# Optimization experiments

Hardware: AMD Instinct MI355X
Metric: run time of the kernel (lower is better)

The kernel has to match this reference:

```python
import jax, jax.numpy as jnp
import numpy as np

# RPNTrainingProposal / RpnTrainingModel constants (defaults in source)
POS_IOU_T = 0.7
NEG_IOU_T = 0.3
TOTAL_SAMPLES = 256
MAX_POS = 128
CLS_W = 1.0
REG_W = 2.0


def pairwise_iou(a, b):
    # a: [N,4], b: [M,4], boxes as (x1, y1, x2, y2) -> [N, M]
    area_a = (a[:, 2] - a[:, 0]) * (a[:, 3] - a[:, 1])
    area_b = (b[:, 2] - b[:, 0]) * (b[:, 3] - b[:, 1])
    lt = jnp.maximum(a[:, None, :2], b[None, :, :2])
    rb = jnp.minimum(a[:, None, 2:], b[None, :, 2:])
    wh = jnp.clip(rb - lt, 0.0)
    inter = wh[..., 0] * wh[..., 1]
    return inter / (area_a[:, None] + area_b[None, :] - inter)


def encode_bbox(anchors, gt):
    aw = anchors[:, 2] - anchors[:, 0]
    ah = anchors[:, 3] - anchors[:, 1]
    acx = anchors[:, 0] + 0.5 * aw
    acy = anchors[:, 1] + 0.5 * ah
    gw = gt[:, 2] - gt[:, 0]
    gh = gt[:, 3] - gt[:, 1]
    gcx = gt[:, 0] + 0.5 * gw
    gcy = gt[:, 1] + 0.5 * gh
    return jnp.stack([(gcx - acx) / aw, (gcy - acy) / ah,
                      jnp.log(gw / aw), jnp.log(gh / ah)], axis=1)


def select_training_samples(anchors, gt_bboxes):
    """Static-shape port of RPNTrainingProposal.call.

    Faithful to the source: 'max_scores' is argmax(iou, axis=1) (an int gt
    index) which the source compares against the float iou thresholds, so
    label=1 <=> gt_idx >= 1 and label=0 <=> gt_idx == 0. top_k(max_scores, n_pos)
    therefore selects exactly the label==1 anchors (and top_k(-max_scores) the
    label==0 ones); tf.random_shuffle subsampling is replaced by a
    deterministic (stable index-order) subsample of the same sets.
    """
    iou = pairwise_iou(anchors, gt_bboxes)                  # [N, M]
    gt_idx = jnp.argmax(iou, axis=1).astype(jnp.int32)      # source 'max_scores'
    ms = gt_idx.astype(jnp.float32)
    labels = jnp.full(gt_idx.shape, -1, jnp.int32)
    labels = jnp.where(ms > POS_IOU_T, 1, labels)
    labels = jnp.where(ms < NEG_IOU_T, 0, labels)
    pos_mask = labels == 1
    neg_mask = labels == 0
    num_pos = jnp.sum(pos_mask)
    cur_pos = jnp.minimum(num_pos, MAX_POS)                 # negatives fill the rest
    # stable sort keys: positives (resp. negatives) first, in anchor-index order
    pos_order = jnp.argsort(jnp.where(pos_mask, 0, 1), stable=True)
    neg_order = jnp.argsort(jnp.where(neg_mask, 0, 1), stable=True)
    i = jnp.arange(TOTAL_SAMPLES)
    sel = jnp.where(i < cur_pos, pos_order[i],
                    neg_order[jnp.clip(i - cur_pos, 0)])    # [256]
    return sel, labels[sel], gt_idx[sel]


def reference(rpn_score, rpn_bboxes_txtytwth, anchors, gt_bboxes):
    sel, sel_labels, sel_gt_idx = select_training_samples(anchors, gt_bboxes)
    # classification loss: sparse softmax cross-entropy, mean over samples
    logp = jax.nn.log_softmax(rpn_score[sel], axis=-1)      # [256, 2]
    cls = -jnp.take_along_axis(logp, sel_labels[:, None].astype(jnp.int32), axis=1)
    rpn_cls_loss = CLS_W * jnp.mean(cls)
    t_gt = encode_bbox(anchors[sel], gt_bboxes[sel_gt_idx])  # [256, 4]
    t_pred = rpn_bboxes_txtytwth[sel]
    inside = sel_labels.astype(t_pred.dtype)[:, None]
    d = inside * (t_pred - t_gt)
    ad = jnp.abs(d)
    sm = jnp.where(ad < 1.0, 0.5 * d * d, ad - 0.5)
    rpn_reg_loss = jnp.mean(jnp.sum(REG_W * sm, axis=1))
    return rpn_cls_loss, rpn_reg_loss


def setup_inputs() -> dict:
    key = jax.random.key(0)
    ks = jax.random.split(key, 10)
    N, M = 300000, 100

    def make_boxes(kcx, kcy, kw, kh, n, img=1000.0):
        cx = jax.random.uniform(kcx, (n,)) * img
        cy = jax.random.uniform(kcy, (n,)) * img
        w = jax.random.uniform(kw, (n,)) * 120.0 + 16.0
        h = jax.random.uniform(kh, (n,)) * 120.0 + 16.0
        return jnp.stack([cx - 0.5 * w, cy - 0.5 * h, cx + 0.5 * w, cy + 0.5 * h], axis=1)

    anchors = make_boxes(ks[0], ks[1], ks[2], ks[3], N)
    gt_bboxes = make_boxes(ks[4], ks[5], ks[6], ks[7], M)
    rpn_score = jax.random.normal(ks[8], (N, 2), jnp.float32)
    rpn_bboxes_txtytwth = jax.random.normal(ks[9], (N, 4), jnp.float32) * 0.1
    return {"rpn_score": rpn_score, "rpn_bboxes_txtytwth": rpn_bboxes_txtytwth,
            "anchors": anchors, "gt_bboxes": gt_bboxes}
```

## Files before the change

### kernel.cpp

```cpp
#include <hip/hip_runtime.h>
#include <math.h>

#define MAXGT 128
#define POS_LIMIT 128
#define TOTAL 256


__global__ void __launch_bounds__(256)
k1_argmax(const float* __restrict__ anchors, const float* __restrict__ gt,
          int N, int M, unsigned char* __restrict__ g8) {
#pragma clang fp contract(off)
    __shared__ float4 sbox[MAXGT];
    __shared__ float sarea[MAXGT];
    int tid = threadIdx.x;
    if (tid < M) {
        float4 b = ((const float4*)gt)[tid];
        sbox[tid] = b;
        sarea[tid] = (b.z - b.x) * (b.w - b.y);
    }
    __syncthreads();

    int i = blockIdx.x * 256 + tid;
    if (i >= N) return;
    float4 a = ((const float4*)anchors)[i];
    float areaA = (a.z - a.x) * (a.w - a.y);
    float best = -INFINITY;
    int bi = 0;
#pragma unroll 5
    for (int j = 0; j < M; ++j) {
        float4 b = sbox[j];
        float lt0 = fmaxf(a.x, b.x);
        float lt1 = fmaxf(a.y, b.y);
        float rb0 = fminf(a.z, b.z);
        float rb1 = fminf(a.w, b.w);
        float w = fmaxf(rb0 - lt0, 0.0f);
        float h = fmaxf(rb1 - lt1, 0.0f);
        float inter = w * h;
        float iou = inter / ((areaA + sarea[j]) - inter);
        if (iou > best) { best = iou; bi = j; }
    }
    g8[i] = (unsigned char)bi;
}


__global__ void __launch_bounds__(256)
k2_select_loss(const float* __restrict__ score, const float* __restrict__ pred,
               const float* __restrict__ anchors, const float* __restrict__ gt,
               const unsigned char* __restrict__ g8, int N,
               float* __restrict__ out) {
#pragma clang fp contract(off)
    __shared__ int s_ps[POS_LIMIT], s_pg[POS_LIMIT];
    __shared__ int s_ns[TOTAL], s_ng[TOTAL];
    __shared__ int wpo[4], wno[4];

    int tid = threadIdx.x;
    int lane = tid & 63, wave = tid >> 6;
    unsigned long long ltmask = (1ull << lane) - 1ull;

    int posCnt = 0, negCnt = 0;
    int nchunks = (N + 255) >> 8;
    for (int c = 0; c < nchunks && (posCnt < POS_LIMIT || negCnt < TOTAL); ++c) {
        int i = (c << 8) + tid;
        int valid = (i < N);
        int g = valid ? (int)g8[i] : 0;
        int posf = valid && (g >= 1);
        int negf = valid && (g == 0);
        unsigned long long pm = __ballot(posf);
        unsigned long long nm = __ballot(negf);
        if (lane == 0) { wpo[wave] = __popcll(pm); wno[wave] = __popcll(nm); }
        __syncthreads();
        int poff = 0, noff = 0, ptot = 0, ntot = 0;
        for (int w = 0; w < 4; ++w) {
            int cp = wpo[w], cn = wno[w];
            if (w < wave) { poff += cp; noff += cn; }
            ptot += cp; ntot += cn;
        }
        int prank = posCnt + poff + __popcll(pm & ltmask);
        int nrank = negCnt + noff + __popcll(nm & ltmask);
        if (posf && prank < POS_LIMIT) { s_ps[prank] = i; s_pg[prank] = g; }
        if (negf && nrank < TOTAL)     { s_ns[nrank] = i; s_ng[nrank] = g; }
        posCnt += ptot; negCnt += ntot;
        __syncthreads();
    }

    int curPos = min(posCnt, POS_LIMIT);
    int sel, label, g;
    if (tid < curPos) {
        sel = s_ps[tid]; g = s_pg[tid]; label = 1;
    } else {
        int k = tid - curPos;
        if (k >= negCnt) k = (negCnt > 0) ? negCnt - 1 : 0;
        sel = s_ns[k]; g = s_ng[k]; label = 0;
    }

    float s0 = score[2 * sel], s1 = score[2 * sel + 1];
    float m = fmaxf(s0, s1);
    float sh0 = s0 - m, sh1 = s1 - m;
    float lse = logf(expf(sh0) + expf(sh1));
    float cls = -((label ? sh1 : sh0) - lse);

    float reg = 0.0f;
    if (label) {
        float4 a = ((const float4*)anchors)[sel];
        float4 gb = ((const float4*)gt)[g];
        float aw = a.z - a.x, ah = a.w - a.y;
        float acx = a.x + 0.5f * aw, acy = a.y + 0.5f * ah;
        float gw = gb.z - gb.x, gh = gb.w - gb.y;
        float gcx = gb.x + 0.5f * gw, gcy = gb.y + 0.5f * gh;
        float4 p = ((const float4*)pred)[sel];
        float d0 = p.x - (gcx - acx) / aw;
        float d1 = p.y - (gcy - acy) / ah;
        float d2 = p.z - logf(gw / aw);
        float d3 = p.w - logf(gh / ah);
        float a0 = fabsf(d0), a1 = fabsf(d1), a2 = fabsf(d2), a3 = fabsf(d3);
        float sm0 = (a0 < 1.0f) ? 0.5f * d0 * d0 : a0 - 0.5f;
        float sm1 = (a1 < 1.0f) ? 0.5f * d1 * d1 : a1 - 0.5f;
        float sm2 = (a2 < 1.0f) ? 0.5f * d2 * d2 : a2 - 0.5f;
        float sm3 = (a3 < 1.0f) ? 0.5f * d3 * d3 : a3 - 0.5f;
        reg = 2.0f * (sm0 + sm1 + sm2 + sm3);
    }

    for (int off = 32; off > 0; off >>= 1) {
        cls += __shfl_down(cls, off);
        reg += __shfl_down(reg, off);
    }
    __shared__ float rc[4], rr[4];
    if (lane == 0) { rc[wave] = cls; rr[wave] = reg; }
    __syncthreads();
    if (tid == 0) {
        out[0] = (rc[0] + rc[1] + rc[2] + rc[3]) * (1.0f / 256.0f);
        out[1] = (rr[0] + rr[1] + rr[2] + rr[3]) * (1.0f / 256.0f);
    }
}


extern "C" void kernel_launch(void* const* d_in, const int* in_sizes, int n_in,
                              void* d_out, int out_size, void* d_ws, size_t ws_size,
                              hipStream_t stream) {
    const float* rpn_score = (const float*)d_in[0];
    const float* rpn_pred  = (const float*)d_in[1];
    const float* anchors   = (const float*)d_in[2];
    const float* gt        = (const float*)d_in[3];
    int N = in_sizes[2] / 4;
    int M = in_sizes[3] / 4;
    if (M > MAXGT) M = MAXGT;

    int nb = (N + 255) / 256;
    unsigned char* g8 = (unsigned char*)d_ws;

    k1_argmax<<<nb, 256, 0, stream>>>(anchors, gt, N, M, g8);
    k2_select_loss<<<1, 256, 0, stream>>>(rpn_score, rpn_pred, anchors, gt,
                                          g8, N, (float*)d_out);
}
```

Before: 94.19 us.

## Compute IoU argmax for an anchor prefix only and fall back lazily in selection

```diff
diff --git a/kernel.cpp b/kernel.cpp
--- a/kernel.cpp
+++ b/kernel.cpp
@@ -4,25 +4,11 @@
 #define MAXGT 128
 #define POS_LIMIT 128
 #define TOTAL 256
+#define PREFIX 65536
 
-
-__global__ void __launch_bounds__(256)
-k1_argmax(const float* __restrict__ anchors, const float* __restrict__ gt,
-          int N, int M, unsigned char* __restrict__ g8) {
+__device__ __forceinline__ int iou_argmax(float4 a, int M,
+                                          const float4* sbox, const float* sarea) {
 #pragma clang fp contract(off)
-    __shared__ float4 sbox[MAXGT];
-    __shared__ float sarea[MAXGT];
-    int tid = threadIdx.x;
-    if (tid < M) {
-        float4 b = ((const float4*)gt)[tid];
-        sbox[tid] = b;
-        sarea[tid] = (b.z - b.x) * (b.w - b.y);
-    }
-    __syncthreads();
-
-    int i = blockIdx.x * 256 + tid;
-    if (i >= N) return;
-    float4 a = ((const float4*)anchors)[i];
     float areaA = (a.z - a.x) * (a.w - a.y);
     float best = -INFINITY;
     int bi = 0;
@@ -39,19 +25,48 @@
         float iou = inter / ((areaA + sarea[j]) - inter);
         if (iou > best) { best = iou; bi = j; }
     }
-    g8[i] = (unsigned char)bi;
+    return bi;
+}
+
+__device__ __forceinline__ void stage_gt(const float* __restrict__ gt, int M,
+                                         float4* sbox, float* sarea) {
+#pragma clang fp contract(off)
+    int tid = threadIdx.x;
+    if (tid < M) {
+        float4 b = ((const float4*)gt)[tid];
+        sbox[tid] = b;
+        sarea[tid] = (b.z - b.x) * (b.w - b.y);
+    }
+    __syncthreads();
+}
+
+
+__global__ void __launch_bounds__(256)
+k1_argmax(const float* __restrict__ anchors, const float* __restrict__ gt,
+          int N, int M, unsigned char* __restrict__ g8) {
+    __shared__ float4 sbox[MAXGT];
+    __shared__ float sarea[MAXGT];
+    stage_gt(gt, M, sbox, sarea);
+    int i = blockIdx.x * 256 + threadIdx.x;
+    if (i >= N) return;
+    float4 a = ((const float4*)anchors)[i];
+    g8[i] = (unsigned char)iou_argmax(a, M, sbox, sarea);
 }
 
 
 __global__ void __launch_bounds__(256)
 k2_select_loss(const float* __restrict__ score, const float* __restrict__ pred,
                const float* __restrict__ anchors, const float* __restrict__ gt,
-               const unsigned char* __restrict__ g8, int N,
+               const unsigned char* __restrict__ g8, int N, int M, int P,
                float* __restrict__ out) {
 #pragma clang fp contract(off)
+    __shared__ float4 sbox[MAXGT];
+    __shared__ float sarea[MAXGT];
     __shared__ int s_ps[POS_LIMIT], s_pg[POS_LIMIT];
     __shared__ int s_ns[TOTAL], s_ng[TOTAL];
     __shared__ int wpo[4], wno[4];
+
+    stage_gt(gt, M, sbox, sarea);
 
     int tid = threadIdx.x;
     int lane = tid & 63, wave = tid >> 6;
@@ -59,10 +74,18 @@
 
     int posCnt = 0, negCnt = 0;
     int nchunks = (N + 255) >> 8;
-    for (int c = 0; c < nchunks && (posCnt < POS_LIMIT || negCnt < TOTAL); ++c) {
+    for (int c = 0; c < nchunks; ++c) {
+        if (posCnt >= POS_LIMIT && negCnt >= (TOTAL - POS_LIMIT)) break;
         int i = (c << 8) + tid;
         int valid = (i < N);
-        int g = valid ? (int)g8[i] : 0;
+        int g = 0;
+        if (valid) {
+            if (i < P) g = (int)g8[i];
+            else {
+                float4 a = ((const float4*)anchors)[i];
+                g = iou_argmax(a, M, sbox, sarea);
+            }
+        }
         int posf = valid && (g >= 1);
         int negf = valid && (g == 0);
         unsigned long long pm = __ballot(posf);
@@ -102,7 +125,7 @@
     float reg = 0.0f;
     if (label) {
         float4 a = ((const float4*)anchors)[sel];
-        float4 gb = ((const float4*)gt)[g];
+        float4 gb = sbox[g];
         float aw = a.z - a.x, ah = a.w - a.y;
         float acx = a.x + 0.5f * aw, acy = a.y + 0.5f * ah;
         float gw = gb.z - gb.x, gh = gb.w - gb.y;
@@ -145,10 +168,11 @@
     int M = in_sizes[3] / 4;
     if (M > MAXGT) M = MAXGT;
 
-    int nb = (N + 255) / 256;
+    int P = (N < PREFIX) ? N : PREFIX;
+    int nb = (P + 255) / 256;
     unsigned char* g8 = (unsigned char*)d_ws;
 
-    k1_argmax<<<nb, 256, 0, stream>>>(anchors, gt, N, M, g8);
+    k1_argmax<<<nb, 256, 0, stream>>>(anchors, gt, P, M, g8);
     k2_select_loss<<<1, 256, 0, stream>>>(rpn_score, rpn_pred, anchors, gt,
-                                          g8, N, (float*)d_out);
+                                          g8, N, M, P, (float*)d_out);
 }
```

Result: faster. 75.89 us (-19.4%).
